# Kernel tuning notes

Measured on AMD Instinct MI355X. Metric: run time of the kernel, lower is better.

Reference implementation:

```python
import jax, jax.numpy as jnp
import numpy as np

N, K, R = 32768, 4096, 256

def setup_inputs() -> dict:
    key = jax.random.key(0)
    k1, k2, k3 = jax.random.split(key, 3)
    H = jax.random.normal(k1, (N, R), dtype=jnp.float32)
    L = jax.random.normal(k2, (K, R), dtype=jnp.float32)
    W_I = jax.random.normal(k3, (R, R), dtype=jnp.float32)
    return {"H": H, "L": L, "W_I": W_I}

def reference(H, L, W_I):
    # Q = W_I @ L^T : (r, k)
    Q = jnp.einsum('rs,ks->rk', W_I, L)
    # M_I = H @ Q : (n, k)
    M_I = jnp.einsum('nr,rk->nk', H, Q)
    A_I = jax.nn.softmax(M_I, axis=1)
    # C_I = A_I @ L : (n, r)
    C_I = jnp.einsum('nk,kr->nr', A_I, L)
    return (C_I, A_I)
```

## Files before the change

kernel.cpp:

```cpp
#include <hip/hip_runtime.h>
#include <hip/hip_bf16.h>
#include <math.h>
#include <stdint.h>

constexpr int N_ROWS = 32768;
constexpr int K_DIM  = 4096;
constexpr int R_DIM  = 256;
constexpr int KP     = 3 * R_DIM;

typedef __bf16 bf16x8 __attribute__((ext_vector_type(8)));
typedef float  f32x4  __attribute__((ext_vector_type(4)));
typedef unsigned short u16x8 __attribute__((ext_vector_type(8)));

__device__ __forceinline__ unsigned short f2bf(float x) {
    unsigned u = __float_as_uint(x);
    u += 0x7fffu + ((u >> 16) & 1u);
    return (unsigned short)(u >> 16);
}
__device__ __forceinline__ float bf2f(unsigned short h) {
    return __uint_as_float((unsigned)h << 16);
}

__device__ __forceinline__ void gl2lds16(const void* gptr, void* lptr) {
    __builtin_amdgcn_global_load_lds(
        (const __attribute__((address_space(1))) unsigned int*)gptr,
        (__attribute__((address_space(3))) unsigned int*)lptr,
        16, 0, 0);
}

__global__ __launch_bounds__(256)
void gemm_mfma_nt(const unsigned short* __restrict__ A,
                  const unsigned short* __restrict__ B,
                  float* __restrict__ C, int M, int N, int Kc)
{
    __shared__ __align__(16) unsigned short As[128 * 32];
    __shared__ __align__(16) unsigned short Bs[128 * 32];

    const int tid  = threadIdx.x;
    const int wave = tid >> 6, lane = tid & 63;
    const int wm = wave >> 1, wn = wave & 1;
    const long m0 = (long)blockIdx.x * 128;
    const long n0 = (long)blockIdx.y * 128;

    f32x4 acc[4][4] = {};

    const int srow  = lane >> 2;
    const int skoff = (lane & 3) * 8;
    const int c0 = wave, c1 = wave + 4;
    const int kq = (lane >> 4) * 8;
    const int mr = lane & 15;

    for (int k0 = 0; k0 < Kc; k0 += 32) {
        gl2lds16(A + (m0 + c0 * 16 + srow) * (long)Kc + k0 + skoff, &As[c0 * 512]);
        gl2lds16(A + (m0 + c1 * 16 + srow) * (long)Kc + k0 + skoff, &As[c1 * 512]);
        gl2lds16(B + (n0 + c0 * 16 + srow) * (long)Kc + k0 + skoff, &Bs[c0 * 512]);
        gl2lds16(B + (n0 + c1 * 16 + srow) * (long)Kc + k0 + skoff, &Bs[c1 * 512]);
        __syncthreads();

        bf16x8 af[4], bfr[4];
#pragma unroll
        for (int t = 0; t < 4; ++t) {
            af[t]  = *(const bf16x8*)&As[(wm * 64 + t * 16 + mr) * 32 + kq];
            bfr[t] = *(const bf16x8*)&Bs[(wn * 64 + t * 16 + mr) * 32 + kq];
        }
#pragma unroll
        for (int i = 0; i < 4; ++i)
#pragma unroll
            for (int j = 0; j < 4; ++j)
                acc[i][j] = __builtin_amdgcn_mfma_f32_16x16x32_bf16(
                    af[i], bfr[j], acc[i][j], 0, 0, 0);
        __syncthreads();
    }

    const int col = lane & 15, rquad = (lane >> 4) * 4;
#pragma unroll
    for (int i = 0; i < 4; ++i) {
        const long mrow = m0 + wm * 64 + i * 16 + rquad;
#pragma unroll
        for (int j = 0; j < 4; ++j) {
            float* p = C + mrow * (long)N + n0 + wn * 64 + j * 16 + col;
#pragma unroll
            for (int r = 0; r < 4; ++r) p[(long)r * N] = acc[i][j][r];
        }
    }
}

__global__ __launch_bounds__(256)
void gemm_mfma_a32(const float* __restrict__ A,
                   const unsigned short* __restrict__ B,
                   float* __restrict__ C, int M, int N, int Kc)
{
    __shared__ __align__(16) unsigned short As[128 * 32];
    __shared__ __align__(16) unsigned short Bs[128 * 32];

    const int tid  = threadIdx.x;
    const int wave = tid >> 6, lane = tid & 63;
    const int wm = wave >> 1, wn = wave & 1;
    const long m0 = (long)blockIdx.x * 128;
    const long n0 = (long)blockIdx.y * 128;

    f32x4 acc[4][4] = {};

    const int srow  = lane >> 2;
    const int skoff = (lane & 3) * 8;
    const int c0 = wave, c1 = wave + 4;
    const int kq = (lane >> 4) * 8;
    const int mr = lane & 15;

    const int arow  = tid >> 1;
    const int ahalf = (tid & 1) * 16;

    for (int k0 = 0; k0 < Kc; k0 += 32) {
        gl2lds16(B + (n0 + c0 * 16 + srow) * (long)Kc + k0 + skoff, &Bs[c0 * 512]);
        gl2lds16(B + (n0 + c1 * 16 + srow) * (long)Kc + k0 + skoff, &Bs[c1 * 512]);
        {
            const float* g = A + (m0 + arow) * (long)Kc + k0 + ahalf;
            float4 v0 = *(const float4*)(g + 0);
            float4 v1 = *(const float4*)(g + 4);
            float4 v2 = *(const float4*)(g + 8);
            float4 v3 = *(const float4*)(g + 12);
            u16x8 u0, u1;
            u0[0] = f2bf(v0.x); u0[1] = f2bf(v0.y); u0[2] = f2bf(v0.z); u0[3] = f2bf(v0.w);
            u0[4] = f2bf(v1.x); u0[5] = f2bf(v1.y); u0[6] = f2bf(v1.z); u0[7] = f2bf(v1.w);
            u1[0] = f2bf(v2.x); u1[1] = f2bf(v2.y); u1[2] = f2bf(v2.z); u1[3] = f2bf(v2.w);
            u1[4] = f2bf(v3.x); u1[5] = f2bf(v3.y); u1[6] = f2bf(v3.z); u1[7] = f2bf(v3.w);
            *(u16x8*)&As[arow * 32 + ahalf + 0] = u0;
            *(u16x8*)&As[arow * 32 + ahalf + 8] = u1;
        }
        __syncthreads();

        bf16x8 af[4], bfr[4];
#pragma unroll
        for (int t = 0; t < 4; ++t) {
            af[t]  = *(const bf16x8*)&As[(wm * 64 + t * 16 + mr) * 32 + kq];
            bfr[t] = *(const bf16x8*)&Bs[(wn * 64 + t * 16 + mr) * 32 + kq];
        }
#pragma unroll
        for (int i = 0; i < 4; ++i)
#pragma unroll
            for (int j = 0; j < 4; ++j)
                acc[i][j] = __builtin_amdgcn_mfma_f32_16x16x32_bf16(
                    af[i], bfr[j], acc[i][j], 0, 0, 0);
        __syncthreads();
    }

    const int col = lane & 15, rquad = (lane >> 4) * 4;
#pragma unroll
    for (int i = 0; i < 4; ++i) {
        const long mrow = m0 + wm * 64 + i * 16 + rquad;
#pragma unroll
        for (int j = 0; j < 4; ++j) {
            float* p = C + mrow * (long)N + n0 + wn * 64 + j * 16 + col;
#pragma unroll
            for (int r = 0; r < 4; ++r) p[(long)r * N] = acc[i][j][r];
        }
    }
}

__global__ __launch_bounds__(256)
void prep_A(const float* __restrict__ P, unsigned short* __restrict__ Ap)
{
    const long i = (long)blockIdx.x * 256 + threadIdx.x;
    const long n = i >> 8; const int r = (int)(i & 255);
    const float x = P[i];
    const unsigned short hi = f2bf(x);
    const unsigned short lo = f2bf(x - bf2f(hi));
    unsigned short* row = Ap + n * KP;
    row[r] = hi; row[R_DIM + r] = hi; row[2 * R_DIM + r] = lo;
}

__global__ __launch_bounds__(256)
void prep_B(const float* __restrict__ L, unsigned short* __restrict__ Bp)
{
    const long i = (long)blockIdx.x * 256 + threadIdx.x;
    const long k = i >> 8; const int r = (int)(i & 255);
    const float x = L[i];
    const unsigned short hi = f2bf(x);
    const unsigned short lo = f2bf(x - bf2f(hi));
    unsigned short* row = Bp + k * KP;
    row[r] = hi; row[R_DIM + r] = lo; row[2 * R_DIM + r] = hi;
}

__global__ __launch_bounds__(256)
void prep_LT(const float* __restrict__ L, unsigned short* __restrict__ LT)
{
    const long i = (long)blockIdx.x * 256 + threadIdx.x;
    const long r = i >> 12; const long k = i & 4095;
    LT[r * K_DIM + k] = f2bf(L[k * R_DIM + r]);
}

template<bool BT>
__global__ __launch_bounds__(256)
void gemm128(const float* __restrict__ A, const float* __restrict__ B,
             float* __restrict__ C, int M, int N, int Kc)
{
    __shared__ __align__(16) float Asl[16][132];
    __shared__ __align__(16) float Bsl[16][132];

    const int tid = threadIdx.x;
    const int tx = tid & 15, ty = tid >> 4;
    const long m0 = (long)blockIdx.x * 128;
    const long n0 = (long)blockIdx.y * 128;

    float acc[8][8];
#pragma unroll
    for (int i = 0; i < 8; ++i)
#pragma unroll
        for (int j = 0; j < 8; ++j) acc[i][j] = 0.f;

    for (int k0 = 0; k0 < Kc; k0 += 16) {
#pragma unroll
        for (int q = 0; q < 2; ++q) {
            int fi = tid + 256 * q, row = fi >> 2, col = (fi & 3) * 4;
            float4 v = *(const float4*)(A + (m0 + row) * (long)Kc + k0 + col);
            Asl[col + 0][row] = v.x; Asl[col + 1][row] = v.y;
            Asl[col + 2][row] = v.z; Asl[col + 3][row] = v.w;
        }
        if (BT) {
#pragma unroll
            for (int q = 0; q < 2; ++q) {
                int fi = tid + 256 * q, row = fi >> 2, col = (fi & 3) * 4;
                float4 v = *(const float4*)(B + (n0 + row) * (long)Kc + k0 + col);
                Bsl[col + 0][row] = v.x; Bsl[col + 1][row] = v.y;
                Bsl[col + 2][row] = v.z; Bsl[col + 3][row] = v.w;
            }
        } else {
#pragma unroll
            for (int q = 0; q < 2; ++q) {
                int fi = tid + 256 * q, row = fi >> 5, col = (fi & 31) * 4;
                float4 v = *(const float4*)(B + (k0 + row) * (long)N + n0 + col);
                *(float4*)&Bsl[row][col] = v;
            }
        }
        __syncthreads();
#pragma unroll
        for (int kk = 0; kk < 16; ++kk) {
            float a[8], b[8];
            *(float4*)&a[0] = *(const float4*)&Asl[kk][ty * 8];
            *(float4*)&a[4] = *(const float4*)&Asl[kk][ty * 8 + 4];
            *(float4*)&b[0] = *(const float4*)&Bsl[kk][tx * 8];
            *(float4*)&b[4] = *(const float4*)&Bsl[kk][tx * 8 + 4];
#pragma unroll
            for (int i = 0; i < 8; ++i)
#pragma unroll
                for (int j = 0; j < 8; ++j)
                    acc[i][j] = fmaf(a[i], b[j], acc[i][j]);
        }
        __syncthreads();
    }
#pragma unroll
    for (int i = 0; i < 8; ++i) {
        float* p = C + (m0 + ty * 8 + i) * (long)N + n0 + tx * 8;
        *(float4*)p       = make_float4(acc[i][0], acc[i][1], acc[i][2], acc[i][3]);
        *(float4*)(p + 4) = make_float4(acc[i][4], acc[i][5], acc[i][6], acc[i][7]);
    }
}

__global__ __launch_bounds__(256)
void softmax_rows(float* __restrict__ Mio)
{
    const long n  = blockIdx.x;
    float* row    = Mio + n * (long)K_DIM;
    const int tid = threadIdx.x;

    float4 v[4];
    float lmax = -3.4e38f;
#pragma unroll
    for (int q = 0; q < 4; ++q) {
        v[q] = ((const float4*)row)[tid + 256 * q];
        lmax = fmaxf(lmax, fmaxf(fmaxf(v[q].x, v[q].y), fmaxf(v[q].z, v[q].w)));
    }
    __shared__ float redmax[4], redsum[4];
#pragma unroll
    for (int off = 32; off > 0; off >>= 1)
        lmax = fmaxf(lmax, __shfl_xor(lmax, off));
    if ((tid & 63) == 0) redmax[tid >> 6] = lmax;
    __syncthreads();
    const float gmax = fmaxf(fmaxf(redmax[0], redmax[1]), fmaxf(redmax[2], redmax[3]));

    float lsum = 0.f;
#pragma unroll
    for (int q = 0; q < 4; ++q) {
        v[q].x = __expf(v[q].x - gmax); v[q].y = __expf(v[q].y - gmax);
        v[q].z = __expf(v[q].z - gmax); v[q].w = __expf(v[q].w - gmax);
        lsum += v[q].x + v[q].y + v[q].z + v[q].w;
    }
#pragma unroll
    for (int off = 32; off > 0; off >>= 1)
        lsum += __shfl_xor(lsum, off);
    if ((tid & 63) == 0) redsum[tid >> 6] = lsum;
    __syncthreads();
    const float inv = 1.f / (redsum[0] + redsum[1] + redsum[2] + redsum[3]);
#pragma unroll
    for (int q = 0; q < 4; ++q) {
        v[q].x *= inv; v[q].y *= inv; v[q].z *= inv; v[q].w *= inv;
        ((float4*)row)[tid + 256 * q] = v[q];
    }
}

extern "C" void kernel_launch(void* const* d_in, const int* in_sizes, int n_in,
                              void* d_out, int out_size, void* d_ws, size_t ws_size,
                              hipStream_t stream)
{
    const float* H  = (const float*)d_in[0];
    const float* L  = (const float*)d_in[1];
    const float* Wi = (const float*)d_in[2];

    float* Cout = (float*)d_out;
    float* Aout = (float*)d_out + (size_t)N_ROWS * R_DIM;

    const size_t szAp = (size_t)N_ROWS * KP * 2;
    const size_t szBp = (size_t)K_DIM * KP * 2;
    const size_t szLT = (size_t)R_DIM * K_DIM * 2;

    if (ws_size >= szAp + szBp + szLT) {
        unsigned short* Ap = (unsigned short*)d_ws;
        unsigned short* Bp = (unsigned short*)((char*)d_ws + szAp);
        unsigned short* LT = (unsigned short*)((char*)d_ws + szAp + szBp);

        gemm128<false><<<dim3(N_ROWS / 128, R_DIM / 128), 256, 0, stream>>>(
            H, Wi, Cout, N_ROWS, R_DIM, R_DIM);
        prep_A<<<dim3((N_ROWS * R_DIM) / 256), 256, 0, stream>>>(Cout, Ap);
        prep_B<<<dim3((K_DIM * R_DIM) / 256), 256, 0, stream>>>(L, Bp);
        prep_LT<<<dim3((R_DIM * K_DIM) / 256), 256, 0, stream>>>(L, LT);
        gemm_mfma_nt<<<dim3(N_ROWS / 128, K_DIM / 128), 256, 0, stream>>>(
            Ap, Bp, Aout, N_ROWS, K_DIM, KP);
        softmax_rows<<<dim3(N_ROWS), 256, 0, stream>>>(Aout);
        gemm_mfma_a32<<<dim3(N_ROWS / 128, R_DIM / 128), 256, 0, stream>>>(
            Aout, LT, Cout, N_ROWS, R_DIM, K_DIM);
    } else {
        gemm128<false><<<dim3(N_ROWS / 128, R_DIM / 128), 256, 0, stream>>>(
            H, Wi, Cout, N_ROWS, R_DIM, R_DIM);
        gemm128<true><<<dim3(N_ROWS / 128, K_DIM / 128), 256, 0, stream>>>(
            Cout, L, Aout, N_ROWS, K_DIM, R_DIM);
        softmax_rows<<<dim3(N_ROWS), 256, 0, stream>>>(Aout);
        gemm128<false><<<dim3(N_ROWS / 128, R_DIM / 128), 256, 0, stream>>>(
            Aout, L, Cout, N_ROWS, R_DIM, K_DIM);
    }
}
```

Baseline: 1.281 ms.

## Fuse softmax stats into logits GEMM and softmax normalization into final GEMM

The logits GEMM now emits per-tile row max and sum-of-exp partials in its epilogue. A small kernel combines these into per-row max and inverse sum. A new fused kernel reads raw logits, normalizes them, writes A_I back and feeds bf16 values straight into the MFMA GEMM with L. This drops the separate softmax pass, which read and wrote the full 512MB logits matrix once more. In exchange the final GEMM uses smaller 32-row tiles that reload all of LT per block, and the grid swap changes tile scheduling order.

After: 1.430 ms. 1.12x slower.

```diff
diff --git a/kernel.cpp b/kernel.cpp
--- a/kernel.cpp
+++ b/kernel.cpp
@@ -11,6 +11,7 @@
 typedef __bf16 bf16x8 __attribute__((ext_vector_type(8)));
 typedef float  f32x4  __attribute__((ext_vector_type(4)));
 typedef unsigned short u16x8 __attribute__((ext_vector_type(8)));
+typedef unsigned short u16x4 __attribute__((ext_vector_type(4)));
 
 __device__ __forceinline__ unsigned short f2bf(float x) {
     unsigned u = __float_as_uint(x);
@@ -28,10 +29,12 @@
         16, 0, 0);
 }
 
+template<bool STATS>
 __global__ __launch_bounds__(256)
 void gemm_mfma_nt(const unsigned short* __restrict__ A,
                   const unsigned short* __restrict__ B,
-                  float* __restrict__ C, int M, int N, int Kc)
+                  float* __restrict__ C, int M, int N, int Kc,
+                  float* __restrict__ partM, float* __restrict__ partL)
 {
     __shared__ __align__(16) unsigned short As[128 * 32];
     __shared__ __align__(16) unsigned short Bs[128 * 32];
@@ -39,8 +42,8 @@
     const int tid  = threadIdx.x;
     const int wave = tid >> 6, lane = tid & 63;
     const int wm = wave >> 1, wn = wave & 1;
-    const long m0 = (long)blockIdx.x * 128;
-    const long n0 = (long)blockIdx.y * 128;
+    const long m0 = (long)blockIdx.y * 128;
+    const long n0 = (long)blockIdx.x * 128;
 
     f32x4 acc[4][4] = {};
 
@@ -83,6 +86,147 @@
             for (int r = 0; r < 4; ++r) p[(long)r * N] = acc[i][j][r];
         }
     }
+
+    if constexpr (STATS) {
+        __shared__ float sm[2][128];
+        __shared__ float sl[2][128];
+        float mx[4][4];
+#pragma unroll
+        for (int i = 0; i < 4; ++i)
+#pragma unroll
+            for (int r = 0; r < 4; ++r) {
+                float m_ = fmaxf(fmaxf(acc[i][0][r], acc[i][1][r]),
+                                 fmaxf(acc[i][2][r], acc[i][3][r]));
+#pragma unroll
+                for (int off = 1; off < 16; off <<= 1)
+                    m_ = fmaxf(m_, __shfl_xor(m_, off));
+                mx[i][r] = m_;
+            }
+        if ((lane & 15) == 0) {
+#pragma unroll
+            for (int i = 0; i < 4; ++i)
+#pragma unroll
+                for (int r = 0; r < 4; ++r)
+                    sm[wn][wm * 64 + i * 16 + rquad + r] = mx[i][r];
+        }
+        __syncthreads();
+        float sx[4][4];
+#pragma unroll
+        for (int i = 0; i < 4; ++i)
+#pragma unroll
+            for (int r = 0; r < 4; ++r) {
+                const int row = wm * 64 + i * 16 + rquad + r;
+                const float mc = fmaxf(sm[0][row], sm[1][row]);
+                float s_ = __expf(acc[i][0][r] - mc) + __expf(acc[i][1][r] - mc)
+                         + __expf(acc[i][2][r] - mc) + __expf(acc[i][3][r] - mc);
+#pragma unroll
+                for (int off = 1; off < 16; off <<= 1)
+                    s_ += __shfl_xor(s_, off);
+                sx[i][r] = s_; mx[i][r] = mc;
+            }
+        if ((lane & 15) == 0) {
+#pragma unroll
+            for (int i = 0; i < 4; ++i)
+#pragma unroll
+                for (int r = 0; r < 4; ++r)
+                    sl[wn][wm * 64 + i * 16 + rquad + r] = sx[i][r];
+        }
+        __syncthreads();
+        if (wn == 0 && (lane & 15) == 0) {
+#pragma unroll
+            for (int i = 0; i < 4; ++i)
+#pragma unroll
+                for (int r = 0; r < 4; ++r) {
+                    const int row = wm * 64 + i * 16 + rquad + r;
+                    const long g = (m0 + row) * 32 + blockIdx.x;
+                    partM[g] = mx[i][r];
+                    partL[g] = sl[0][row] + sl[1][row];
+                }
+        }
+    }
+}
+
+__global__ __launch_bounds__(256)
+void stats_combine(const float* __restrict__ partM, const float* __restrict__ partL,
+                   float* __restrict__ rowM, float* __restrict__ rowInv)
+{
+    const int row = blockIdx.x * 256 + threadIdx.x;
+    const float* pm = partM + (long)row * 32;
+    const float* pl = partL + (long)row * 32;
+    float m = -3.4e38f;
+#pragma unroll
+    for (int i = 0; i < 32; ++i) m = fmaxf(m, pm[i]);
+    float L = 0.f;
+#pragma unroll
+    for (int i = 0; i < 32; ++i) L += pl[i] * __expf(pm[i] - m);
+    rowM[row] = m;
+    rowInv[row] = 1.f / L;
+}
+
+__global__ __launch_bounds__(256)
+void fused_aw(float* __restrict__ Mio, const unsigned short* __restrict__ LT,
+              const float* __restrict__ rowM, const float* __restrict__ rowInv,
+              float* __restrict__ C)
+{
+    __shared__ __align__(16) unsigned short As[32 * 32];
+    __shared__ __align__(16) unsigned short Bs[256 * 32];
+
+    const int tid = threadIdx.x, wave = tid >> 6, lane = tid & 63;
+    const long m0 = (long)blockIdx.x * 32;
+
+    const int arow = tid >> 3;
+    const int acol = (tid & 7) * 4;
+    const float rm = rowM[m0 + arow];
+    const float ri = rowInv[m0 + arow];
+    float* Mrow = Mio + (m0 + arow) * (long)K_DIM + acol;
+
+    const int srow = lane >> 2, skoff = (lane & 3) * 8;
+    const int kq = (lane >> 4) * 8, mr = lane & 15;
+
+    f32x4 acc[2][4] = {};
+
+    for (int k0 = 0; k0 < K_DIM; k0 += 32) {
+#pragma unroll
+        for (int c4 = 0; c4 < 4; ++c4) {
+            const int c = wave * 4 + c4;
+            gl2lds16(LT + (c * 16 + srow) * (long)K_DIM + k0 + skoff, &Bs[c * 512]);
+        }
+        float4 v = *(const float4*)(Mrow + k0);
+        float4 a;
+        a.x = __expf(v.x - rm) * ri;
+        a.y = __expf(v.y - rm) * ri;
+        a.z = __expf(v.z - rm) * ri;
+        a.w = __expf(v.w - rm) * ri;
+        *(float4*)(Mrow + k0) = a;
+        u16x4 u;
+        u[0] = f2bf(a.x); u[1] = f2bf(a.y); u[2] = f2bf(a.z); u[3] = f2bf(a.w);
+        *(u16x4*)&As[arow * 32 + acol] = u;
+        __syncthreads();
+
+        bf16x8 af[2], bfr[4];
+        af[0] = *(const bf16x8*)&As[(mr) * 32 + kq];
+        af[1] = *(const bf16x8*)&As[(16 + mr) * 32 + kq];
+#pragma unroll
+        for (int j = 0; j < 4; ++j)
+            bfr[j] = *(const bf16x8*)&Bs[(wave * 64 + j * 16 + mr) * 32 + kq];
+#pragma unroll
+        for (int i = 0; i < 2; ++i)
+#pragma unroll
+            for (int j = 0; j < 4; ++j)
+                acc[i][j] = __builtin_amdgcn_mfma_f32_16x16x32_bf16(
+                    af[i], bfr[j], acc[i][j], 0, 0, 0);
+        __syncthreads();
+    }
+
+    const int col = lane & 15, rq = (lane >> 4) * 4;
+#pragma unroll
+    for (int i = 0; i < 2; ++i)
+#pragma unroll
+        for (int j = 0; j < 4; ++j)
+#pragma unroll
+            for (int r = 0; r < 4; ++r)
+                C[(m0 + i * 16 + rq + r) * (long)R_DIM + wave * 64 + j * 16 + col]
+                    = acc[i][j][r];
 }
 
 __global__ __launch_bounds__(256)
@@ -96,19 +240,14 @@
     const int tid  = threadIdx.x;
     const int wave = tid >> 6, lane = tid & 63;
     const int wm = wave >> 1, wn = wave & 1;
-    const long m0 = (long)blockIdx.x * 128;
-    const long n0 = (long)blockIdx.y * 128;
+    const long m0 = (long)blockIdx.y * 128;
+    const long n0 = (long)blockIdx.x * 128;
 
     f32x4 acc[4][4] = {};
-
-    const int srow  = lane >> 2;
-    const int skoff = (lane & 3) * 8;
+    const int srow  = lane >> 2, skoff = (lane & 3) * 8;
     const int c0 = wave, c1 = wave + 4;
-    const int kq = (lane >> 4) * 8;
-    const int mr = lane & 15;
-
-    const int arow  = tid >> 1;
-    const int ahalf = (tid & 1) * 16;
+    const int kq = (lane >> 4) * 8, mr = lane & 15;
+    const int arow = tid >> 1, ahalf = (tid & 1) * 16;
 
     for (int k0 = 0; k0 < Kc; k0 += 32) {
         gl2lds16(B + (n0 + c0 * 16 + srow) * (long)Kc + k0 + skoff, &Bs[c0 * 512]);
@@ -128,7 +267,6 @@
             *(u16x8*)&As[arow * 32 + ahalf + 8] = u1;
         }
         __syncthreads();
-
         bf16x8 af[4], bfr[4];
 #pragma unroll
         for (int t = 0; t < 4; ++t) {
@@ -143,7 +281,6 @@
                     af[i], bfr[j], acc[i][j], 0, 0, 0);
         __syncthreads();
     }
-
     const int col = lane & 15, rquad = (lane >> 4) * 4;
 #pragma unroll
     for (int i = 0; i < 4; ++i) {
@@ -196,18 +333,15 @@
 {
     __shared__ __align__(16) float Asl[16][132];
     __shared__ __align__(16) float Bsl[16][132];
-
     const int tid = threadIdx.x;
     const int tx = tid & 15, ty = tid >> 4;
     const long m0 = (long)blockIdx.x * 128;
     const long n0 = (long)blockIdx.y * 128;
-
     float acc[8][8];
 #pragma unroll
     for (int i = 0; i < 8; ++i)
 #pragma unroll
         for (int j = 0; j < 8; ++j) acc[i][j] = 0.f;
-
     for (int k0 = 0; k0 < Kc; k0 += 16) {
 #pragma unroll
         for (int q = 0; q < 2; ++q) {
@@ -262,7 +396,6 @@
     const long n  = blockIdx.x;
     float* row    = Mio + n * (long)K_DIM;
     const int tid = threadIdx.x;
-
     float4 v[4];
     float lmax = -3.4e38f;
 #pragma unroll
@@ -277,7 +410,6 @@
     if ((tid & 63) == 0) redmax[tid >> 6] = lmax;
     __syncthreads();
     const float gmax = fmaxf(fmaxf(redmax[0], redmax[1]), fmaxf(redmax[2], redmax[3]));
-
     float lsum = 0.f;
 #pragma unroll
     for (int q = 0; q < 4; ++q) {
@@ -312,21 +444,43 @@
     const size_t szAp = (size_t)N_ROWS * KP * 2;
     const size_t szBp = (size_t)K_DIM * KP * 2;
     const size_t szLT = (size_t)R_DIM * K_DIM * 2;
-
-    if (ws_size >= szAp + szBp + szLT) {
-        unsigned short* Ap = (unsigned short*)d_ws;
-        unsigned short* Bp = (unsigned short*)((char*)d_ws + szAp);
-        unsigned short* LT = (unsigned short*)((char*)d_ws + szAp + szBp);
+    const size_t szPM = (size_t)N_ROWS * 32 * 4;
+    const size_t szRM = (size_t)N_ROWS * 4;
+
+    if (ws_size >= szAp + szBp + szLT + 2 * szPM + 2 * szRM) {
+        char* w = (char*)d_ws;
+        unsigned short* Ap = (unsigned short*)w;             w += szAp;
+        unsigned short* Bp = (unsigned short*)w;             w += szBp;
+        unsigned short* LT = (unsigned short*)w;             w += szLT;
+        float* partM  = (float*)w;                           w += szPM;
+        float* partL  = (float*)w;                           w += szPM;
+        float* rowM   = (float*)w;                           w += szRM;
+        float* rowInv = (float*)w;
 
         gemm128<false><<<dim3(N_ROWS / 128, R_DIM / 128), 256, 0, stream>>>(
             H, Wi, Cout, N_ROWS, R_DIM, R_DIM);
         prep_A<<<dim3((N_ROWS * R_DIM) / 256), 256, 0, stream>>>(Cout, Ap);
         prep_B<<<dim3((K_DIM * R_DIM) / 256), 256, 0, stream>>>(L, Bp);
         prep_LT<<<dim3((R_DIM * K_DIM) / 256), 256, 0, stream>>>(L, LT);
-        gemm_mfma_nt<<<dim3(N_ROWS / 128, K_DIM / 128), 256, 0, stream>>>(
-            Ap, Bp, Aout, N_ROWS, K_DIM, KP);
+        gemm_mfma_nt<true><<<dim3(K_DIM / 128, N_ROWS / 128), 256, 0, stream>>>(
+            Ap, Bp, Aout, N_ROWS, K_DIM, KP, partM, partL);
+        stats_combine<<<dim3(N_ROWS / 256), 256, 0, stream>>>(
+            partM, partL, rowM, rowInv);
+        fused_aw<<<dim3(N_ROWS / 32), 256, 0, stream>>>(
+            Aout, LT, rowM, rowInv, Cout);
+    } else if (ws_size >= szAp + szBp + szLT) {
+        unsigned short* Ap = (unsigned short*)d_ws;
+        unsigned short* Bp = (unsigned short*)((char*)d_ws + szAp);
+        unsigned short* LT = (unsigned short*)((char*)d_ws + szAp + szBp);
+        gemm128<false><<<dim3(N_ROWS / 128, R_DIM / 128), 256, 0, stream>>>(
+            H, Wi, Cout, N_ROWS, R_DIM, R_DIM);
+        prep_A<<<dim3((N_ROWS * R_DIM) / 256), 256, 0, stream>>>(Cout, Ap);
+        prep_B<<<dim3((K_DIM * R_DIM) / 256), 256, 0, stream>>>(L, Bp);
+        prep_LT<<<dim3((R_DIM * K_DIM) / 256), 256, 0, stream>>>(L, LT);
+        gemm_mfma_nt<false><<<dim3(K_DIM / 128, N_ROWS / 128), 256, 0, stream>>>(
+            Ap, Bp, Aout, N_ROWS, K_DIM, KP, nullptr, nullptr);
         softmax_rows<<<dim3(N_ROWS), 256, 0, stream>>>(Aout);
-        gemm_mfma_a32<<<dim3(N_ROWS / 128, R_DIM / 128), 256, 0, stream>>>(
+        gemm_mfma_a32<<<dim3(R_DIM / 128, N_ROWS / 128), 256, 0, stream>>>(
             Aout, LT, Cout, N_ROWS, R_DIM, K_DIM);
     } else {
         gemm128<false><<<dim3(N_ROWS / 128, R_DIM / 128), 256, 0, stream>>>(
```
